# Optimization experiments

Measured on AMD Instinct MI355X. Metric: run time of the kernel, lower is better.

Reference implementation:

```python
import jax, jax.numpy as jnp
import numpy as np

N = 16777216
PRIOR_SIGMA = 1.0
LOG_SQRT_2PI = 0.5 * float(np.log(2.0 * np.pi))


def gaussian_log_prob(x, mu, sigma):
    # log N(x; mu, sigma) = -log(sigma) - 0.5*log(2*pi) - 0.5*((x-mu)/sigma)^2
    z = (x - mu) / sigma
    return -jnp.log(sigma) - LOG_SQRT_2PI - 0.5 * z * z


def setup_inputs() -> dict:
    key = jax.random.key(0)
    k1, k2, k3, k4, k5, k6 = jax.random.split(key, 6)
    noisy_weights = jax.random.normal(k1, (N,), dtype=jnp.float32)
    mu_weights = jax.random.normal(k2, (N,), dtype=jnp.float32)
    # strictly positive sigmas in [0.5, 1.5)
    sigma_weights = jax.random.uniform(k3, (N,), dtype=jnp.float32) + 0.5
    mu_prediction = jax.random.normal(k4, (), dtype=jnp.float32)
    sigma_prediction = jax.random.uniform(k5, (), dtype=jnp.float32) + 0.5
    y_true = jax.random.normal(k6, (), dtype=jnp.float32)
    return {
        "noisy_weights": noisy_weights,
        "mu_weights": mu_weights,
        "sigma_weights": sigma_weights,
        "mu_prediction": mu_prediction,
        "sigma_prediction": sigma_prediction,
        "y_true": y_true,
    }


def reference(noisy_weights, mu_weights, sigma_weights, mu_prediction, sigma_prediction, y_true):
    # log q(w) under the fully-factorized variational Gaussian (vectorized over all weights)
    loss_variational = gaussian_log_prob(noisy_weights, mu_weights, sigma_weights).sum()
    # log p(w) under the zero-mean isotropic Gaussian prior
    loss_prior = gaussian_log_prob(noisy_weights, jnp.float32(0.0), jnp.float32(PRIOR_SIGMA)).sum()
    # log p(y | prediction)
    loss_likelihood = gaussian_log_prob(y_true, mu_prediction, sigma_prediction)
    return loss_variational - loss_prior - loss_likelihood
```

## Files before the change

### kernel.cpp

```cpp
#include <hip/hip_runtime.h>
#include <math.h>

#define NBLK  2048
#define BLKSZ 256

#define LOG_SQRT_2PI 0.9189385332046727f

__global__ __launch_bounds__(BLKSZ) void bbb_reduce_kernel(
    const float* __restrict__ x,
    const float* __restrict__ mu,
    const float* __restrict__ sg,
    float* __restrict__ partials,
    int n4)
{
    const int tid    = blockIdx.x * BLKSZ + threadIdx.x;
    const int stride = gridDim.x * BLKSZ;

    const float4* __restrict__ x4 = reinterpret_cast<const float4*>(x);
    const float4* __restrict__ m4 = reinterpret_cast<const float4*>(mu);
    const float4* __restrict__ s4 = reinterpret_cast<const float4*>(sg);

    float acc = 0.0f;
    for (int i = tid; i < n4; i += stride) {
        float4 xv = x4[i];
        float4 mv = m4[i];
        float4 sv = s4[i];

        const float xs[4] = {xv.x, xv.y, xv.z, xv.w};
        const float ms[4] = {mv.x, mv.y, mv.z, mv.w};
        const float ss[4] = {sv.x, sv.y, sv.z, sv.w};

        #pragma unroll
        for (int j = 0; j < 4; ++j) {
            float xx = xs[j];
            float rs = __builtin_amdgcn_rcpf(ss[j]);
            float z  = (xx - ms[j]) * rs;
            acc += 0.5f * (xx * xx - z * z) - __logf(ss[j]);
        }
    }

    #pragma unroll
    for (int o = 32; o > 0; o >>= 1)
        acc += __shfl_down(acc, o, 64);

    __shared__ float wsum[BLKSZ / 64];
    const int lane = threadIdx.x & 63;
    const int wid  = threadIdx.x >> 6;
    if (lane == 0) wsum[wid] = acc;
    __syncthreads();

    if (threadIdx.x == 0) {
        float s = 0.0f;
        #pragma unroll
        for (int w = 0; w < BLKSZ / 64; ++w) s += wsum[w];
        partials[blockIdx.x] = s;
    }
}

__global__ __launch_bounds__(BLKSZ) void bbb_final_kernel(
    const float* __restrict__ partials,
    const float* __restrict__ mu_pred,
    const float* __restrict__ sg_pred,
    const float* __restrict__ y_true,
    float* __restrict__ out)
{
    float acc = 0.0f;
    for (int i = threadIdx.x; i < NBLK; i += BLKSZ)
        acc += partials[i];

    #pragma unroll
    for (int o = 32; o > 0; o >>= 1)
        acc += __shfl_down(acc, o, 64);

    __shared__ float wsum[BLKSZ / 64];
    const int lane = threadIdx.x & 63;
    const int wid  = threadIdx.x >> 6;
    if (lane == 0) wsum[wid] = acc;
    __syncthreads();

    if (threadIdx.x == 0) {
        float s = 0.0f;
        #pragma unroll
        for (int w = 0; w < BLKSZ / 64; ++w) s += wsum[w];

        float mp = mu_pred[0];
        float sp = sg_pred[0];
        float y  = y_true[0];
        float zp = (y - mp) / sp;
        float lik = -logf(sp) - LOG_SQRT_2PI - 0.5f * zp * zp;
        out[0] = s - lik;
    }
}

extern "C" void kernel_launch(void* const* d_in, const int* in_sizes, int n_in,
                              void* d_out, int out_size, void* d_ws, size_t ws_size,
                              hipStream_t stream) {
    const float* noisy = (const float*)d_in[0];
    const float* mu    = (const float*)d_in[1];
    const float* sigma = (const float*)d_in[2];
    const float* mu_p  = (const float*)d_in[3];
    const float* sg_p  = (const float*)d_in[4];
    const float* y_t   = (const float*)d_in[5];

    float* partials = (float*)d_ws;
    float* out      = (float*)d_out;

    const int n  = in_sizes[0];
    const int n4 = n / 4;

    bbb_reduce_kernel<<<NBLK, BLKSZ, 0, stream>>>(noisy, mu, sigma, partials, n4);
    bbb_final_kernel<<<1, BLKSZ, 0, stream>>>(partials, mu_p, sg_p, y_t, out);
}
```

Before: 38.82 us.

## Batch eight float4 loads per thread and fold logs into one product

Replaces the grid-stride loop with a fixed grid in which each thread issues eight float4 loads per input before computing, so more memory requests are in flight. The per-element log is replaced by accumulating the product of 32 sigmas and taking one log at the end, which cuts transcendental work. The grid is now sized from n (2048 blocks for this n), so the final kernel takes the block count as a parameter. The product of 32 sigmas in [0.5,1.5) could underflow or overflow in extreme cases and slightly changes rounding.

```diff
diff --git a/kernel.cpp b/kernel.cpp
--- a/kernel.cpp
+++ b/kernel.cpp
@@ -1,8 +1,8 @@
 #include <hip/hip_runtime.h>
 #include <math.h>
 
-#define NBLK  2048
 #define BLKSZ 256
+#define ITER  8
 
 #define LOG_SQRT_2PI 0.9189385332046727f
 
@@ -13,29 +13,55 @@
     float* __restrict__ partials,
     int n4)
 {
-    const int tid    = blockIdx.x * BLKSZ + threadIdx.x;
-    const int stride = gridDim.x * BLKSZ;
+    const int tid = threadIdx.x;
+    const long long base = (long long)blockIdx.x * (BLKSZ * ITER) + tid;
 
     const float4* __restrict__ x4 = reinterpret_cast<const float4*>(x);
     const float4* __restrict__ m4 = reinterpret_cast<const float4*>(mu);
     const float4* __restrict__ s4 = reinterpret_cast<const float4*>(sg);
 
-    float acc = 0.0f;
-    for (int i = tid; i < n4; i += stride) {
-        float4 xv = x4[i];
-        float4 mv = m4[i];
-        float4 sv = s4[i];
+    float acc  = 0.0f;
+    float prod = 1.0f;
 
-        const float xs[4] = {xv.x, xv.y, xv.z, xv.w};
-        const float ms[4] = {mv.x, mv.y, mv.z, mv.w};
-        const float ss[4] = {sv.x, sv.y, sv.z, sv.w};
+    if (base + (long long)(ITER - 1) * BLKSZ < n4) {
+        float4 xv[ITER], mv[ITER], sv[ITER];
+        #pragma unroll
+        for (int k = 0; k < ITER; ++k) xv[k] = x4[base + (long long)k * BLKSZ];
+        #pragma unroll
+        for (int k = 0; k < ITER; ++k) mv[k] = m4[base + (long long)k * BLKSZ];
+        #pragma unroll
+        for (int k = 0; k < ITER; ++k) sv[k] = s4[base + (long long)k * BLKSZ];
 
         #pragma unroll
-        for (int j = 0; j < 4; ++j) {
-            float xx = xs[j];
-            float rs = __builtin_amdgcn_rcpf(ss[j]);
-            float z  = (xx - ms[j]) * rs;
-            acc += 0.5f * (xx * xx - z * z) - __logf(ss[j]);
+        for (int k = 0; k < ITER; ++k) {
+            const float xs[4] = {xv[k].x, xv[k].y, xv[k].z, xv[k].w};
+            const float ms[4] = {mv[k].x, mv[k].y, mv[k].z, mv[k].w};
+            const float ss[4] = {sv[k].x, sv[k].y, sv[k].z, sv[k].w};
+            #pragma unroll
+            for (int j = 0; j < 4; ++j) {
+                float xx = xs[j];
+                float rs = __builtin_amdgcn_rcpf(ss[j]);
+                float z  = (xx - ms[j]) * rs;
+                acc  += 0.5f * (xx * xx - z * z);
+                prod *= ss[j];
+            }
+        }
+        acc -= __logf(prod);
+    } else {
+        #pragma unroll
+        for (int k = 0; k < ITER; ++k) {
+            long long i = base + (long long)k * BLKSZ;
+            if (i < n4) {
+                float4 xv = x4[i], mv = m4[i], sv = s4[i];
+                const float xs[4] = {xv.x, xv.y, xv.z, xv.w};
+                const float ms[4] = {mv.x, mv.y, mv.z, mv.w};
+                const float ss[4] = {sv.x, sv.y, sv.z, sv.w};
+                for (int j = 0; j < 4; ++j) {
+                    float rs = __builtin_amdgcn_rcpf(ss[j]);
+                    float z  = (xs[j] - ms[j]) * rs;
+                    acc += 0.5f * (xs[j] * xs[j] - z * z) - __logf(ss[j]);
+                }
+            }
         }
     }
 
@@ -62,10 +88,11 @@
     const float* __restrict__ mu_pred,
     const float* __restrict__ sg_pred,
     const float* __restrict__ y_true,
-    float* __restrict__ out)
+    float* __restrict__ out,
+    int nblk)
 {
     float acc = 0.0f;
-    for (int i = threadIdx.x; i < NBLK; i += BLKSZ)
+    for (int i = threadIdx.x; i < nblk; i += BLKSZ)
         acc += partials[i];
 
     #pragma unroll
@@ -107,7 +134,8 @@
 
     const int n  = in_sizes[0];
     const int n4 = n / 4;
+    const int nblk = (n4 + BLKSZ * ITER - 1) / (BLKSZ * ITER);
 
-    bbb_reduce_kernel<<<NBLK, BLKSZ, 0, stream>>>(noisy, mu, sigma, partials, n4);
-    bbb_final_kernel<<<1, BLKSZ, 0, stream>>>(partials, mu_p, sg_p, y_t, out);
+    bbb_reduce_kernel<<<nblk, BLKSZ, 0, stream>>>(noisy, mu, sigma, partials, n4);
+    bbb_final_kernel<<<1, BLKSZ, 0, stream>>>(partials, mu_p, sg_p, y_t, out, nblk);
 }
```

New measurement: 36.64 us. 5.6% less time.
